# Kernel tuning notes

Measured on AMD Instinct MI355X. Metric: run time of the kernel, lower is better.

The kernel has to match this reference:

```python
import jax, jax.numpy as jnp
import numpy as np

NEG_SLOPE = 0.2  # PyG GATConv default leaky_relu slope
EPS = 1e-16


def gat_conv(x, W, att_src, att_dst, bias, src, dst, num_nodes, heads, out_ch, concat):
    # x: [N, F_in]; W: [F_in, heads*out_ch]
    h = (x @ W).reshape(num_nodes, heads, out_ch)          # [N, H, C]
    a_src = jnp.sum(h * att_src, axis=-1)                  # [N, H]
    a_dst = jnp.sum(h * att_dst, axis=-1)                  # [N, H]
    alpha = jax.nn.leaky_relu(a_src[src] + a_dst[dst], NEG_SLOPE)  # [E, H]
    # segment softmax over incoming edges of each destination node
    amax = jax.ops.segment_max(alpha, dst, num_segments=num_nodes)  # [N, H]
    ex = jnp.exp(alpha - amax[dst])                        # [E, H]
    denom = jax.ops.segment_sum(ex, dst, num_segments=num_nodes)    # [N, H]
    attn = ex / (denom[dst] + EPS)                         # [E, H]
    msg = h[src] * attn[:, :, None]                        # [E, H, C]
    out = jax.ops.segment_sum(msg, dst, num_segments=num_nodes)     # [N, H, C]
    if concat:
        out = out.reshape(num_nodes, heads * out_ch)
    else:
        out = out.mean(axis=1)
    return out + bias


def setup_inputs() -> dict:
    key = jax.random.key(0)
    ks = jax.random.split(key, 10)
    N, E, F_in, H, C, OUT = 50000, 800000, 512, 4, 64, 40
    x = jax.random.normal(ks[0], (N, F_in), dtype=jnp.float32)
    edge_index = jax.random.randint(ks[1], (2, E), 0, N, dtype=jnp.int64)
    s1 = (2.0 / (F_in + H * C)) ** 0.5
    s2 = (2.0 / (H * C + OUT)) ** 0.5
    return {
        "x": x,
        "edge_index": edge_index,
        "W1": jax.random.normal(ks[2], (F_in, H * C), dtype=jnp.float32) * s1,
        "att_src1": jax.random.normal(ks[3], (H, C), dtype=jnp.float32) * 0.1,
        "att_dst1": jax.random.normal(ks[4], (H, C), dtype=jnp.float32) * 0.1,
        "b1": jnp.zeros((H * C,), dtype=jnp.float32),
        "W2": jax.random.normal(ks[5], (H * C, OUT), dtype=jnp.float32) * s2,
        "att_src2": jax.random.normal(ks[6], (1, OUT), dtype=jnp.float32) * 0.1,
        "att_dst2": jax.random.normal(ks[7], (1, OUT), dtype=jnp.float32) * 0.1,
        "b2": jnp.zeros((OUT,), dtype=jnp.float32),
    }


def reference(x, edge_index, W1, att_src1, att_dst1, b1, W2, att_src2, att_dst2, b2):
    N = x.shape[0]
    H, C = att_src1.shape
    OUT = att_src2.shape[1]
    # PyG GATConv default: add self-loops
    loops = jnp.arange(N, dtype=edge_index.dtype)
    src = jnp.concatenate([edge_index[0], loops])
    dst = jnp.concatenate([edge_index[1], loops])
    # dropout is identity in eval mode
    h = gat_conv(x, W1, att_src1, att_dst1, b1, src, dst, N, H, C, concat=True)
    h = jax.nn.elu(h)
    out = gat_conv(h, W2, att_src2, att_dst2, b2, src, dst, N, 1, OUT, concat=False)
    return jax.nn.log_softmax(out, axis=1)
```

## Files before the change

### kernel.cpp

```cpp
#include <hip/hip_runtime.h>
#include <math.h>

#define FIN   512
#define H1DIM 256
#define HEADS 4
#define CH    64
#define OUTC  40
#define NEG   0.2f
#define EPSV  1e-16f
#define BK    64

__device__ __forceinline__ float leaky(float a) { return fmaxf(a, NEG * a); }

__device__ __forceinline__ short f2bf(float f) {
    unsigned u = __builtin_bit_cast(unsigned, f);
    u += 0x7FFFu + ((u >> 16) & 1u);
    return (short)(u >> 16);
}
__device__ __forceinline__ float bf2f(short s) {
    return __builtin_bit_cast(float, ((unsigned)(unsigned short)s) << 16);
}
__device__ __forceinline__ unsigned cvtpk(float lo, float hi) {
    unsigned r;
    asm("v_cvt_pk_bf16_f32 %0, %1, %2" : "=v"(r) : "v"(lo), "v"(hi));
    return r;
}
__device__ __forceinline__ float lo16(unsigned u) {
    return __builtin_bit_cast(float, u << 16);
}
__device__ __forceinline__ float hi16(unsigned u) {
    return __builtin_bit_cast(float, u & 0xffff0000u);
}

typedef __attribute__((ext_vector_type(2))) float floatx2;

__device__ __forceinline__ unsigned f32x2_to_fp8x2(float a, float b) {
    return (unsigned)__builtin_amdgcn_cvt_pk_fp8_f32(a, b, 0, false);
}
template <bool HI>
__device__ __forceinline__ floatx2 fp8x2_to_f32(unsigned u) {
    return __builtin_amdgcn_cvt_pk_f32_fp8((int)u, HI);
}

typedef __attribute__((ext_vector_type(8))) short short8;
typedef __attribute__((ext_vector_type(4))) short short4_t;
typedef __attribute__((ext_vector_type(4))) float float4_t;

typedef unsigned int u32;
typedef const __attribute__((address_space(1))) u32 gu32;
typedef __attribute__((address_space(3))) u32 lu32;

__device__ __forceinline__ void load_lds16(const void* g, void* l) {
    __builtin_amdgcn_global_load_lds((gu32*)g, (lu32*)l, 16, 0, 0);
}

__global__ void cvt_w1_kernel(const float* __restrict__ W1, short* __restrict__ w1t)
{
    int idx = blockIdx.x * 256 + threadIdx.x;
    if (idx >= FIN * H1DIM) return;
    int k = idx >> 8;
    int n = idx & 255;
    w1t[(size_t)n * FIN + k] = f2bf(W1[idx]);
}

__global__ __launch_bounds__(256) void gemm1_mfma_kernel(
    const float* __restrict__ x, const short* __restrict__ w1t,
    const float* __restrict__ attS, const float* __restrict__ attD,
    unsigned char* __restrict__ h1f, float* __restrict__ aS1, float* __restrict__ aD1, int N)
{
    __shared__ float Alf[64 * BK];
    __shared__ short Bls[256 * BK];

    const int tid  = threadIdx.x;
    const int lane = tid & 63;
    const int wid  = tid >> 6;
    const int row0 = blockIdx.x * 64;
    const int col0 = wid * 64;
    const int quad = lane >> 4;
    const int m16  = lane & 15;

    const int achunk = ((tid & 15) ^ (tid >> 4)) * 4;
    const float* asrcA[4];
#pragma unroll
    for (int p = 0; p < 4; ++p) {
        int r = row0 + p * 16 + (tid >> 4);
        if (r >= N) r = N - 1;
        asrcA[p] = x + (size_t)r * FIN + achunk;
    }

    const int trow = tid >> 3;
    const int bswz = ((tid & 7) ^ (trow & 7)) * 8;
    const short* bsrc[8];
#pragma unroll
    for (int p = 0; p < 8; ++p)
        bsrc[p] = w1t + (size_t)(p * 32 + trow) * FIN + bswz;

    float4_t acc[4][4];
#pragma unroll
    for (int i = 0; i < 4; ++i)
#pragma unroll
        for (int j = 0; j < 4; ++j) acc[i][j] = (float4_t){0.f, 0.f, 0.f, 0.f};

    const int swzB = (m16 & 7);

    for (int k0 = 0; k0 < FIN; k0 += BK) {
#pragma unroll
        for (int p = 0; p < 4; ++p)
            load_lds16(asrcA[p] + k0, Alf + p * 1024 + tid * 4);
#pragma unroll
        for (int p = 0; p < 8; ++p)
            load_lds16(bsrc[p] + k0, Bls + p * 2048 + tid * 8);
        __syncthreads();

#pragma unroll
        for (int half = 0; half < 2; ++half) {
            short8 a[4], b[4];
#pragma unroll
            for (int i = 0; i < 4; ++i) {
                int row = i * 16 + m16;
                int c0 = (quad + 4 * half) * 2;
                float4 f0 = *(const float4*)&Alf[row * BK + ((c0 ^ m16) * 4)];
                float4 f1 = *(const float4*)&Alf[row * BK + (((c0 + 1) ^ m16) * 4)];
                unsigned* tp = (unsigned*)&a[i];
                tp[0] = cvtpk(f0.x, f0.y);
                tp[1] = cvtpk(f0.z, f0.w);
                tp[2] = cvtpk(f1.x, f1.y);
                tp[3] = cvtpk(f1.z, f1.w);
            }
#pragma unroll
            for (int j = 0; j < 4; ++j) {
                int col = col0 + j * 16 + m16;
                int sub = (quad + 4 * half) ^ swzB;
                b[j] = *(const short8*)&Bls[col * BK + sub * 8];
            }
#pragma unroll
            for (int i = 0; i < 4; ++i)
#pragma unroll
                for (int j = 0; j < 4; ++j)
                    acc[i][j] = __builtin_amdgcn_mfma_f32_16x16x32_bf16(a[i], b[j], acc[i][j], 0, 0, 0);
        }
        __syncthreads();
    }

    float attSv[4], attDv[4];
#pragma unroll
    for (int j = 0; j < 4; ++j) {
        attSv[j] = attS[col0 + j * 16 + m16];
        attDv[j] = attD[col0 + j * 16 + m16];
    }

#pragma unroll
    for (int i = 0; i < 4; ++i) {
#pragma unroll
        for (int r = 0; r < 4; ++r) {
            int row = row0 + i * 16 + quad * 4 + r;
            if (row < N) {
                unsigned pa = f32x2_to_fp8x2(acc[i][0][r], acc[i][1][r]);
                unsigned pb = f32x2_to_fp8x2(acc[i][2][r], acc[i][3][r]);
                unsigned char* hp = h1f + (size_t)row * H1DIM + col0 + m16;
                hp[0]  = (unsigned char)(pa & 0xff);
                hp[16] = (unsigned char)((pa >> 8) & 0xff);
                hp[32] = (unsigned char)(pb & 0xff);
                hp[48] = (unsigned char)((pb >> 8) & 0xff);
            }
            float ps = acc[i][0][r] * attSv[0] + acc[i][1][r] * attSv[1]
                     + acc[i][2][r] * attSv[2] + acc[i][3][r] * attSv[3];
            float pd = acc[i][0][r] * attDv[0] + acc[i][1][r] * attDv[1]
                     + acc[i][2][r] * attDv[2] + acc[i][3][r] * attDv[3];
#pragma unroll
            for (int off = 1; off < 16; off <<= 1) {
                ps += __shfl_xor(ps, off);
                pd += __shfl_xor(pd, off);
            }
            if (m16 == 0 && row < N) {
                aS1[(size_t)row * 4 + wid] = ps;
                aD1[(size_t)row * 4 + wid] = pd;
            }
        }
    }
}

__global__ void degcount_kernel(const int* __restrict__ ei, int* __restrict__ deg,
                                int* __restrict__ rank, int E, int Etot)
{
    int e = blockIdx.x * 256 + threadIdx.x;
    if (e >= Etot) return;
    int d = (e < E) ? ei[E + e] : (e - E);
    rank[e] = atomicAdd(&deg[d], 1);
}

__global__ __launch_bounds__(1024) void scan_partial_kernel(
    const int* __restrict__ deg, int* __restrict__ offsets,
    int* __restrict__ bsums, int N)
{
    __shared__ int wsums[16];
    __shared__ int excl[16];
    int tid = threadIdx.x, lane = tid & 63, wid = tid >> 6;
    int idx = blockIdx.x * 1024 + tid;
    int v = (idx < N) ? deg[idx] : 0;
    int sv = v;
#pragma unroll
    for (int off = 1; off < 64; off <<= 1) {
        int t = __shfl_up(sv, off, 64);
        if (lane >= off) sv += t;
    }
    if (lane == 63) wsums[wid] = sv;
    __syncthreads();
    if (wid == 0 && lane < 16) {
        int wv = wsums[lane];
        int sw = wv;
#pragma unroll
        for (int off = 1; off < 16; off <<= 1) {
            int t = __shfl_up(sw, off, 64);
            if (lane >= off) sw += t;
        }
        excl[lane] = sw - wv;
        if (lane == 15) bsums[blockIdx.x] = sw;
    }
    __syncthreads();
    if (idx < N) offsets[idx + 1] = sv + excl[wid];
}

__global__ __launch_bounds__(1024) void scan_tops_kernel(
    int* __restrict__ bsums, int* __restrict__ boffs, int nb)
{
    __shared__ int wsums[16];
    __shared__ int excl[16];
    int tid = threadIdx.x, lane = tid & 63, wid = tid >> 6;
    int v = (tid < nb) ? bsums[tid] : 0;
    int sv = v;
#pragma unroll
    for (int off = 1; off < 64; off <<= 1) {
        int t = __shfl_up(sv, off, 64);
        if (lane >= off) sv += t;
    }
    if (lane == 63) wsums[wid] = sv;
    __syncthreads();
    if (wid == 0 && lane < 16) {
        int wv = wsums[lane];
        int sw = wv;
#pragma unroll
        for (int off = 1; off < 16; off <<= 1) {
            int t = __shfl_up(sw, off, 64);
            if (lane >= off) sw += t;
        }
        excl[lane] = sw - wv;
    }
    __syncthreads();
    if (tid < nb) boffs[tid] = sv + excl[wid] - v;
}

__global__ __launch_bounds__(1024) void scan_add_kernel(
    int* __restrict__ offsets, const int* __restrict__ boffs, int N)
{
    int idx = blockIdx.x * 1024 + threadIdx.x;
    if (idx == 0) offsets[0] = 0;
    if (idx < N) offsets[idx + 1] += boffs[blockIdx.x];
}

__global__ void scatter_kernel(const int* __restrict__ ei, const int* __restrict__ offsets,
                               const int* __restrict__ rank, int* __restrict__ csr_src,
                               int E, int Etot)
{
    int e = blockIdx.x * 256 + threadIdx.x;
    if (e >= Etot) return;
    int s, d;
    if (e < E) { s = ei[e]; d = ei[E + e]; }
    else       { s = e - E; d = s; }
    csr_src[offsets[d] + rank[e]] = s;
}

__global__ __launch_bounds__(256) void agg1_kernel(
    const unsigned char* __restrict__ h1f, const float* __restrict__ aS,
    const float* __restrict__ aD, const int* __restrict__ offsets,
    const int* __restrict__ csr_src, const float* __restrict__ b1,
    short* __restrict__ g1b, int N)
{
    int lane = threadIdx.x & 63, wid = threadIdx.x >> 6;
    int half = lane >> 5;
    int l32  = lane & 31;
    int n = blockIdx.x * 4 + wid;
    if (n >= N) return;
    int start = offsets[n], end = offsets[n + 1];
    int h = l32 >> 3;
    int cbase = l32 * 8;
    float adh = aD[(size_t)n * 4 + h];

    float ac[8];
#pragma unroll
    for (int c = 0; c < 8; ++c) ac[c] = 0.f;
    float denom = 0.f;

    int p = start;
    for (; p + 4 <= end; p += 4) {
        int sA0 = csr_src[p],     sB0 = csr_src[p + 1];
        int sA1 = csr_src[p + 2], sB1 = csr_src[p + 3];
        int s0 = half ? sB0 : sA0;
        int s1 = half ? sB1 : sA1;
        float t0 = aS[(size_t)s0 * 4 + h] + adh;
        float t1 = aS[(size_t)s1 * 4 + h] + adh;
        uint2 r0 = *(const uint2*)&h1f[(size_t)s0 * H1DIM + cbase];
        uint2 r1 = *(const uint2*)&h1f[(size_t)s1 * H1DIM + cbase];
        float w0 = __expf(leaky(t0));
        float w1 = __expf(leaky(t1));
        denom += w0 + w1;
        floatx2 d0a = fp8x2_to_f32<false>(r0.x), d0b = fp8x2_to_f32<true>(r0.x);
        floatx2 d0c = fp8x2_to_f32<false>(r0.y), d0d = fp8x2_to_f32<true>(r0.y);
        floatx2 d1a = fp8x2_to_f32<false>(r1.x), d1b = fp8x2_to_f32<true>(r1.x);
        floatx2 d1c = fp8x2_to_f32<false>(r1.y), d1d = fp8x2_to_f32<true>(r1.y);
        ac[0] += w0 * d0a.x + w1 * d1a.x;
        ac[1] += w0 * d0a.y + w1 * d1a.y;
        ac[2] += w0 * d0b.x + w1 * d1b.x;
        ac[3] += w0 * d0b.y + w1 * d1b.y;
        ac[4] += w0 * d0c.x + w1 * d1c.x;
        ac[5] += w0 * d0c.y + w1 * d1c.y;
        ac[6] += w0 * d0d.x + w1 * d1d.x;
        ac[7] += w0 * d0d.y + w1 * d1d.y;
    }
    for (; p + 2 <= end; p += 2) {
        int sA = csr_src[p], sB = csr_src[p + 1];
        int s = half ? sB : sA;
        float t = aS[(size_t)s * 4 + h] + adh;
        uint2 r = *(const uint2*)&h1f[(size_t)s * H1DIM + cbase];
        float w = __expf(leaky(t));
        denom += w;
        floatx2 da = fp8x2_to_f32<false>(r.x), db = fp8x2_to_f32<true>(r.x);
        floatx2 dc = fp8x2_to_f32<false>(r.y), dd = fp8x2_to_f32<true>(r.y);
        ac[0] += w * da.x; ac[1] += w * da.y;
        ac[2] += w * db.x; ac[3] += w * db.y;
        ac[4] += w * dc.x; ac[5] += w * dc.y;
        ac[6] += w * dd.x; ac[7] += w * dd.y;
    }
    if (p < end) {
        int s = csr_src[p];
        float t = aS[(size_t)s * 4 + h] + adh;
        uint2 r = *(const uint2*)&h1f[(size_t)s * H1DIM + cbase];
        float w = half ? 0.f : __expf(leaky(t));
        denom += w;
        floatx2 da = fp8x2_to_f32<false>(r.x), db = fp8x2_to_f32<true>(r.x);
        floatx2 dc = fp8x2_to_f32<false>(r.y), dd = fp8x2_to_f32<true>(r.y);
        ac[0] += w * da.x; ac[1] += w * da.y;
        ac[2] += w * db.x; ac[3] += w * db.y;
        ac[4] += w * dc.x; ac[5] += w * dc.y;
        ac[6] += w * dd.x; ac[7] += w * dd.y;
    }

    denom += __shfl_xor(denom, 32);
#pragma unroll
    for (int c = 0; c < 8; ++c) ac[c] += __shfl_xor(ac[c], 32);

    if (half == 0) {
        float inv = 1.f / (denom + EPSV);
        float4 b0 = *(const float4*)&b1[cbase];
        float4 b4 = *(const float4*)&b1[cbase + 4];
        float v[8];
        v[0] = ac[0] * inv + b0.x;
        v[1] = ac[1] * inv + b0.y;
        v[2] = ac[2] * inv + b0.z;
        v[3] = ac[3] * inv + b0.w;
        v[4] = ac[4] * inv + b4.x;
        v[5] = ac[5] * inv + b4.y;
        v[6] = ac[6] * inv + b4.z;
        v[7] = ac[7] * inv + b4.w;
#pragma unroll
        for (int c = 0; c < 8; ++c) v[c] = v[c] > 0.f ? v[c] : expm1f(v[c]);
        short8 o;
        unsigned* op = (unsigned*)&o;
        op[0] = cvtpk(v[0], v[1]);
        op[1] = cvtpk(v[2], v[3]);
        op[2] = cvtpk(v[4], v[5]);
        op[3] = cvtpk(v[6], v[7]);
        *(short8*)&g1b[(size_t)n * H1DIM + cbase] = o;
    }
}

__global__ __launch_bounds__(256) void gemm2_kernel(
    const short* __restrict__ g1b, const float* __restrict__ W2,
    const float* __restrict__ attS2, const float* __restrict__ attD2,
    short* __restrict__ h2b, float* __restrict__ aS2, float* __restrict__ aD2, int N)
{
    __shared__ float rows[4][8][256];
    int lane = threadIdx.x & 63, wid = threadIdx.x >> 6;
    int nbase = blockIdx.x * 32 + wid * 8;
    bool act = lane < OUTC;
    int cc = act ? lane : 0;
    float attS = act ? attS2[lane] : 0.f;
    float attD = act ? attD2[lane] : 0.f;

#pragma unroll
    for (int i = 0; i < 8; ++i) {
        int n = nbase + i;
        float4 v = make_float4(0.f, 0.f, 0.f, 0.f);
        if (n < N) {
            short4_t hv = *(const short4_t*)&g1b[(size_t)n * H1DIM + lane * 4];
            v = make_float4(bf2f(hv[0]), bf2f(hv[1]), bf2f(hv[2]), bf2f(hv[3]));
        }
        *(float4*)&rows[wid][i][lane * 4] = v;
    }

    float acc[8];
#pragma unroll
    for (int i = 0; i < 8; ++i) acc[i] = 0.f;

    for (int k = 0; k < H1DIM; k += 4) {
        float w0 = W2[(size_t)(k + 0) * OUTC + cc];
        float w1 = W2[(size_t)(k + 1) * OUTC + cc];
        float w2 = W2[(size_t)(k + 2) * OUTC + cc];
        float w3 = W2[(size_t)(k + 3) * OUTC + cc];
#pragma unroll
        for (int i = 0; i < 8; ++i) {
            float4 g = *(const float4*)&rows[wid][i][k];
            acc[i] += g.x * w0 + g.y * w1 + g.z * w2 + g.w * w3;
        }
    }

#pragma unroll
    for (int i = 0; i < 8; ++i) {
        int n = nbase + i;
        if (n >= N) continue;
        if (act) h2b[(size_t)n * OUTC + lane] = f2bf(acc[i]);
        float ts = act ? acc[i] * attS : 0.f;
        float td = act ? acc[i] * attD : 0.f;
#pragma unroll
        for (int off = 32; off > 0; off >>= 1) {
            ts += __shfl_xor(ts, off);
            td += __shfl_xor(td, off);
        }
        if (lane == 0) { aS2[n] = ts; aD2[n] = td; }
    }
}

__global__ __launch_bounds__(256) void agg2_kernel(
    const short* __restrict__ h2b, const float* __restrict__ aS2,
    const float* __restrict__ aD2, const int* __restrict__ offsets,
    const int* __restrict__ csr_src, const float* __restrict__ b2,
    float* __restrict__ out, int N)
{
    int lane = threadIdx.x & 63, wid = threadIdx.x >> 6;
    int n = blockIdx.x * 4 + wid;
    if (n >= N) return;
    int start = offsets[n], end = offsets[n + 1];
    bool act = lane < OUTC;
    int cc = act ? lane : 0;
    float ad = aD2[n];

    float acc = 0.f, denom = 0.f;
    int p = start;
    for (; p + 4 <= end; p += 4) {
        int s0 = csr_src[p], s1 = csr_src[p + 1], s2 = csr_src[p + 2], s3 = csr_src[p + 3];
        float w0 = __expf(leaky(aS2[s0] + ad));
        float w1 = __expf(leaky(aS2[s1] + ad));
        float w2 = __expf(leaky(aS2[s2] + ad));
        float w3 = __expf(leaky(aS2[s3] + ad));
        short v0 = h2b[(size_t)s0 * OUTC + cc];
        short v1 = h2b[(size_t)s1 * OUTC + cc];
        short v2 = h2b[(size_t)s2 * OUTC + cc];
        short v3 = h2b[(size_t)s3 * OUTC + cc];
        denom += w0 + w1 + w2 + w3;
        acc += w0 * bf2f(v0) + w1 * bf2f(v1) + w2 * bf2f(v2) + w3 * bf2f(v3);
    }
    for (; p < end; ++p) {
        int s = csr_src[p];
        float w = __expf(leaky(aS2[s] + ad));
        denom += w;
        acc += w * bf2f(h2b[(size_t)s * OUTC + cc]);
    }

    float v = acc / (denom + EPSV) + (act ? b2[lane] : 0.f);

    float vm = act ? v : -INFINITY;
#pragma unroll
    for (int off = 32; off > 0; off >>= 1) vm = fmaxf(vm, __shfl_xor(vm, off));
    float ex2 = act ? __expf(v - vm) : 0.f;
    float tot = ex2;
#pragma unroll
    for (int off = 32; off > 0; off >>= 1) tot += __shfl_xor(tot, off);
    float res = v - vm - __logf(tot);
    if (act) out[(size_t)n * OUTC + lane] = res;
}

extern "C" void kernel_launch(void* const* d_in, const int* in_sizes, int n_in,
                              void* d_out, int out_size, void* d_ws, size_t ws_size,
                              hipStream_t stream)
{
    const float* x     = (const float*)d_in[0];
    const int*   ei    = (const int*)d_in[1];
    const float* W1    = (const float*)d_in[2];
    const float* attS1 = (const float*)d_in[3];
    const float* attD1 = (const float*)d_in[4];
    const float* b1    = (const float*)d_in[5];
    const float* W2    = (const float*)d_in[6];
    const float* attS2 = (const float*)d_in[7];
    const float* attD2 = (const float*)d_in[8];
    const float* b2    = (const float*)d_in[9];
    float* out = (float*)d_out;

    const int N    = in_sizes[0] / FIN;
    const int E    = in_sizes[1] / 2;
    const int Etot = E + N;
    const int nb   = (N + 1023) / 1024;

    char* ws = (char*)d_ws;
    size_t off = 0;
    auto take = [&](size_t bytes) -> char* {
        char* p = ws + off;
        off = (off + bytes + 255) & ~(size_t)255;
        return p;
    };
    unsigned char* h1f = (unsigned char*)take((size_t)N * H1DIM);
    short* g1b     = (short*)take((size_t)N * H1DIM * 2);
    short* w1t     = (short*)take((size_t)FIN * H1DIM * 2);
    float* aS1     = (float*)take((size_t)N * 4 * 4);
    float* aD1     = (float*)take((size_t)N * 4 * 4);
    short* h2b     = (short*)take((size_t)N * OUTC * 2);
    float* aS2v    = (float*)take((size_t)N * 4);
    float* aD2v    = (float*)take((size_t)N * 4);
    int*   deg     = (int*)take((size_t)N * 4);
    int*   offsets = (int*)take((size_t)(N + 1) * 4);
    int*   bsums   = (int*)take((size_t)nb * 4);
    int*   boffs   = (int*)take((size_t)nb * 4);
    int*   rank    = (int*)take((size_t)Etot * 4);
    int*   csr_src = (int*)take((size_t)Etot * 4);

    (void)hipMemsetAsync(deg, 0, (size_t)N * 4, stream);

    cvt_w1_kernel<<<(FIN * H1DIM + 255) / 256, 256, 0, stream>>>(W1, w1t);
    gemm1_mfma_kernel<<<(N + 63) / 64, 256, 0, stream>>>(x, w1t, attS1, attD1, h1f, aS1, aD1, N);
    degcount_kernel<<<(Etot + 255) / 256, 256, 0, stream>>>(ei, deg, rank, E, Etot);
    scan_partial_kernel<<<nb, 1024, 0, stream>>>(deg, offsets, bsums, N);
    scan_tops_kernel<<<1, 1024, 0, stream>>>(bsums, boffs, nb);
    scan_add_kernel<<<nb, 1024, 0, stream>>>(offsets, boffs, N);
    scatter_kernel<<<(Etot + 255) / 256, 256, 0, stream>>>(ei, offsets, rank, csr_src, E, Etot);
    agg1_kernel<<<(N + 3) / 4, 256, 0, stream>>>(h1f, aS1, aD1, offsets, csr_src, b1, g1b, N);
    gemm2_kernel<<<(N + 31) / 32, 256, 0, stream>>>(g1b, W2, attS2, attD2, h2b, aS2v, aD2v, N);
    agg2_kernel<<<(N + 3) / 4, 256, 0, stream>>>(h2b, aS2v, aD2v, offsets, csr_src, b2, out, N);
}
```

Before: 389.4 us.

## Double-buffer A tile in LDS and load W1 fragments directly from global

The GEMM1 kernel drops the LDS staging of the bf16 W1 tile. Each lane now loads its B fragments straight from global memory, which W1's small size should keep in L2. The A (x) tile is double-buffered in LDS, with the next tile prefetched before the current one is computed, and manual vmcnt waits plus s_barrier replace __syncthreads. Launch bounds request 4 blocks per CU to raise occupancy, at the risk of register pressure and of uncoalesced B global loads with hand-tuned waitcnt values that must stay exact.

```diff
diff --git a/kernel.cpp b/kernel.cpp
--- a/kernel.cpp
+++ b/kernel.cpp
@@ -63,13 +63,12 @@
     w1t[(size_t)n * FIN + k] = f2bf(W1[idx]);
 }
 
-__global__ __launch_bounds__(256) void gemm1_mfma_kernel(
+__global__ __launch_bounds__(256, 4) void gemm1_mfma_kernel(
     const float* __restrict__ x, const short* __restrict__ w1t,
     const float* __restrict__ attS, const float* __restrict__ attD,
     unsigned char* __restrict__ h1f, float* __restrict__ aS1, float* __restrict__ aD1, int N)
 {
-    __shared__ float Alf[64 * BK];
-    __shared__ short Bls[256 * BK];
+    __shared__ float Alf[2][64 * BK];
 
     const int tid  = threadIdx.x;
     const int lane = tid & 63;
@@ -88,12 +87,10 @@
         asrcA[p] = x + (size_t)r * FIN + achunk;
     }
 
-    const int trow = tid >> 3;
-    const int bswz = ((tid & 7) ^ (trow & 7)) * 8;
-    const short* bsrc[8];
-#pragma unroll
-    for (int p = 0; p < 8; ++p)
-        bsrc[p] = w1t + (size_t)(p * 32 + trow) * FIN + bswz;
+    const short* bp[4];
+#pragma unroll
+    for (int j = 0; j < 4; ++j)
+        bp[j] = w1t + (size_t)(col0 + j * 16 + m16) * FIN + quad * 8;
 
     float4_t acc[4][4];
 #pragma unroll
@@ -101,26 +98,43 @@
 #pragma unroll
         for (int j = 0; j < 4; ++j) acc[i][j] = (float4_t){0.f, 0.f, 0.f, 0.f};
 
-    const int swzB = (m16 & 7);
-
-    for (int k0 = 0; k0 < FIN; k0 += BK) {
-#pragma unroll
-        for (int p = 0; p < 4; ++p)
-            load_lds16(asrcA[p] + k0, Alf + p * 1024 + tid * 4);
-#pragma unroll
-        for (int p = 0; p < 8; ++p)
-            load_lds16(bsrc[p] + k0, Bls + p * 2048 + tid * 8);
-        __syncthreads();
-
+#pragma unroll
+    for (int p = 0; p < 4; ++p)
+        load_lds16(asrcA[p], Alf[0] + p * 1024 + tid * 4);
+
+#pragma unroll
+    for (int kk = 0; kk < FIN / BK; ++kk) {
+        const int k0 = kk * BK;
+
+        short8 b[2][4];
+#pragma unroll
+        for (int half = 0; half < 2; ++half)
+#pragma unroll
+            for (int j = 0; j < 4; ++j)
+                b[half][j] = *(const short8*)(bp[j] + k0 + half * 32);
+
+        if (kk < FIN / BK - 1) {
+#pragma unroll
+            for (int p = 0; p < 4; ++p)
+                load_lds16(asrcA[p] + k0 + BK, Alf[(kk + 1) & 1] + p * 1024 + tid * 4);
+            asm volatile("s_waitcnt vmcnt(12)" ::: "memory");
+        } else {
+            asm volatile("s_waitcnt vmcnt(8)" ::: "memory");
+        }
+        __builtin_amdgcn_sched_barrier(0);
+        __builtin_amdgcn_s_barrier();
+        __builtin_amdgcn_sched_barrier(0);
+
+        const float* Acur = Alf[kk & 1];
 #pragma unroll
         for (int half = 0; half < 2; ++half) {
-            short8 a[4], b[4];
+            short8 a[4];
 #pragma unroll
             for (int i = 0; i < 4; ++i) {
                 int row = i * 16 + m16;
                 int c0 = (quad + 4 * half) * 2;
-                float4 f0 = *(const float4*)&Alf[row * BK + ((c0 ^ m16) * 4)];
-                float4 f1 = *(const float4*)&Alf[row * BK + (((c0 + 1) ^ m16) * 4)];
+                float4 f0 = *(const float4*)&Acur[row * BK + ((c0 ^ m16) * 4)];
+                float4 f1 = *(const float4*)&Acur[row * BK + (((c0 + 1) ^ m16) * 4)];
                 unsigned* tp = (unsigned*)&a[i];
                 tp[0] = cvtpk(f0.x, f0.y);
                 tp[1] = cvtpk(f0.z, f0.w);
@@ -128,18 +142,14 @@
                 tp[3] = cvtpk(f1.z, f1.w);
             }
 #pragma unroll
-            for (int j = 0; j < 4; ++j) {
-                int col = col0 + j * 16 + m16;
-                int sub = (quad + 4 * half) ^ swzB;
-                b[j] = *(const short8*)&Bls[col * BK + sub * 8];
-            }
-#pragma unroll
             for (int i = 0; i < 4; ++i)
 #pragma unroll
                 for (int j = 0; j < 4; ++j)
-                    acc[i][j] = __builtin_amdgcn_mfma_f32_16x16x32_bf16(a[i], b[j], acc[i][j], 0, 0, 0);
-        }
-        __syncthreads();
+                    acc[i][j] = __builtin_amdgcn_mfma_f32_16x16x32_bf16(a[i], b[half][j], acc[i][j], 0, 0, 0);
+        }
+        __builtin_amdgcn_sched_barrier(0);
+        __builtin_amdgcn_s_barrier();
+        __builtin_amdgcn_sched_barrier(0);
     }
 
     float attSv[4], attDv[4];
```

After: 411.1 us. +5.6%, slower.

## Double gemm1 row tile and stage fp8 output through LDS for coalesced stores

Applied to the files above, without the earlier changes.

The first-layer GEMM now computes 128 rows per block instead of 64, so each W1 tile loaded into LDS is reused across twice as many rows and fewer blocks are launched. The A-fragment conversion moves inside the row loop to keep register pressure down, and launch bounds request two blocks per SM. The fp8 outputs are written into an LDS bounce buffer and then stored as 16-byte vector writes instead of scattered single-byte stores. In exchange the kernel uses more accumulator registers and LDS per block, which may lower occupancy, and adds one extra barrier.

```diff
diff --git a/kernel.cpp b/kernel.cpp
--- a/kernel.cpp
+++ b/kernel.cpp
@@ -25,12 +25,6 @@
     asm("v_cvt_pk_bf16_f32 %0, %1, %2" : "=v"(r) : "v"(lo), "v"(hi));
     return r;
 }
-__device__ __forceinline__ float lo16(unsigned u) {
-    return __builtin_bit_cast(float, u << 16);
-}
-__device__ __forceinline__ float hi16(unsigned u) {
-    return __builtin_bit_cast(float, u & 0xffff0000u);
-}
 
 typedef __attribute__((ext_vector_type(2))) float floatx2;
 
@@ -63,26 +57,26 @@
     w1t[(size_t)n * FIN + k] = f2bf(W1[idx]);
 }
 
-__global__ __launch_bounds__(256) void gemm1_mfma_kernel(
+__global__ __launch_bounds__(256, 2) void gemm1_mfma_kernel(
     const float* __restrict__ x, const short* __restrict__ w1t,
     const float* __restrict__ attS, const float* __restrict__ attD,
     unsigned char* __restrict__ h1f, float* __restrict__ aS1, float* __restrict__ aD1, int N)
 {
-    __shared__ float Alf[64 * BK];
+    __shared__ float Alf[128 * BK];
     __shared__ short Bls[256 * BK];
 
     const int tid  = threadIdx.x;
     const int lane = tid & 63;
     const int wid  = tid >> 6;
-    const int row0 = blockIdx.x * 64;
+    const int row0 = blockIdx.x * 128;
     const int col0 = wid * 64;
     const int quad = lane >> 4;
     const int m16  = lane & 15;
 
     const int achunk = ((tid & 15) ^ (tid >> 4)) * 4;
-    const float* asrcA[4];
-#pragma unroll
-    for (int p = 0; p < 4; ++p) {
+    const float* asrcA[8];
+#pragma unroll
+    for (int p = 0; p < 8; ++p) {
         int r = row0 + p * 16 + (tid >> 4);
         if (r >= N) r = N - 1;
         asrcA[p] = x + (size_t)r * FIN + achunk;
@@ -95,9 +89,9 @@
     for (int p = 0; p < 8; ++p)
         bsrc[p] = w1t + (size_t)(p * 32 + trow) * FIN + bswz;
 
-    float4_t acc[4][4];
-#pragma unroll
-    for (int i = 0; i < 4; ++i)
+    float4_t acc[8][4];
+#pragma unroll
+    for (int i = 0; i < 8; ++i)
 #pragma unroll
         for (int j = 0; j < 4; ++j) acc[i][j] = (float4_t){0.f, 0.f, 0.f, 0.f};
 
@@ -105,7 +99,7 @@
 
     for (int k0 = 0; k0 < FIN; k0 += BK) {
 #pragma unroll
-        for (int p = 0; p < 4; ++p)
+        for (int p = 0; p < 8; ++p)
             load_lds16(asrcA[p] + k0, Alf + p * 1024 + tid * 4);
 #pragma unroll
         for (int p = 0; p < 8; ++p)
@@ -114,19 +108,7 @@
 
 #pragma unroll
         for (int half = 0; half < 2; ++half) {
-            short8 a[4], b[4];
-#pragma unroll
-            for (int i = 0; i < 4; ++i) {
-                int row = i * 16 + m16;
-                int c0 = (quad + 4 * half) * 2;
-                float4 f0 = *(const float4*)&Alf[row * BK + ((c0 ^ m16) * 4)];
-                float4 f1 = *(const float4*)&Alf[row * BK + (((c0 + 1) ^ m16) * 4)];
-                unsigned* tp = (unsigned*)&a[i];
-                tp[0] = cvtpk(f0.x, f0.y);
-                tp[1] = cvtpk(f0.z, f0.w);
-                tp[2] = cvtpk(f1.x, f1.y);
-                tp[3] = cvtpk(f1.z, f1.w);
-            }
+            short8 b[4];
 #pragma unroll
             for (int j = 0; j < 4; ++j) {
                 int col = col0 + j * 16 + m16;
@@ -134,10 +116,21 @@
                 b[j] = *(const short8*)&Bls[col * BK + sub * 8];
             }
 #pragma unroll
-            for (int i = 0; i < 4; ++i)
+            for (int i = 0; i < 8; ++i) {
+                int row = i * 16 + m16;
+                int c0 = (quad + 4 * half) * 2;
+                float4 f0 = *(const float4*)&Alf[row * BK + ((c0 ^ m16) * 4)];
+                float4 f1 = *(const float4*)&Alf[row * BK + (((c0 + 1) ^ m16) * 4)];
+                short8 a;
+                unsigned* tp = (unsigned*)&a;
+                tp[0] = cvtpk(f0.x, f0.y);
+                tp[1] = cvtpk(f0.z, f0.w);
+                tp[2] = cvtpk(f1.x, f1.y);
+                tp[3] = cvtpk(f1.z, f1.w);
 #pragma unroll
                 for (int j = 0; j < 4; ++j)
-                    acc[i][j] = __builtin_amdgcn_mfma_f32_16x16x32_bf16(a[i], b[j], acc[i][j], 0, 0, 0);
+                    acc[i][j] = __builtin_amdgcn_mfma_f32_16x16x32_bf16(a, b[j], acc[i][j], 0, 0, 0);
+            }
         }
         __syncthreads();
     }
@@ -149,20 +142,21 @@
         attDv[j] = attD[col0 + j * 16 + m16];
     }
 
-#pragma unroll
-    for (int i = 0; i < 4; ++i) {
+    unsigned char* Bounce = (unsigned char*)Alf;
+
+#pragma unroll
+    for (int i = 0; i < 8; ++i) {
 #pragma unroll
         for (int r = 0; r < 4; ++r) {
-            int row = row0 + i * 16 + quad * 4 + r;
-            if (row < N) {
-                unsigned pa = f32x2_to_fp8x2(acc[i][0][r], acc[i][1][r]);
-                unsigned pb = f32x2_to_fp8x2(acc[i][2][r], acc[i][3][r]);
-                unsigned char* hp = h1f + (size_t)row * H1DIM + col0 + m16;
-                hp[0]  = (unsigned char)(pa & 0xff);
-                hp[16] = (unsigned char)((pa >> 8) & 0xff);
-                hp[32] = (unsigned char)(pb & 0xff);
-                hp[48] = (unsigned char)((pb >> 8) & 0xff);
-            }
+            int rloc = i * 16 + quad * 4 + r;
+            unsigned pa = f32x2_to_fp8x2(acc[i][0][r], acc[i][1][r]);
+            unsigned pb = f32x2_to_fp8x2(acc[i][2][r], acc[i][3][r]);
+            int cb = rloc * 256 + col0 + m16;
+            Bounce[cb]      = (unsigned char)(pa & 0xff);
+            Bounce[cb + 16] = (unsigned char)((pa >> 8) & 0xff);
+            Bounce[cb + 32] = (unsigned char)(pb & 0xff);
+            Bounce[cb + 48] = (unsigned char)((pb >> 8) & 0xff);
+
             float ps = acc[i][0][r] * attSv[0] + acc[i][1][r] * attSv[1]
                      + acc[i][2][r] * attSv[2] + acc[i][3][r] * attSv[3];
             float pd = acc[i][0][r] * attDv[0] + acc[i][1][r] * attDv[1]
@@ -172,11 +166,21 @@
                 ps += __shfl_xor(ps, off);
                 pd += __shfl_xor(pd, off);
             }
+            int row = row0 + rloc;
             if (m16 == 0 && row < N) {
                 aS1[(size_t)row * 4 + wid] = ps;
                 aD1[(size_t)row * 4 + wid] = pd;
             }
         }
+    }
+    __syncthreads();
+
+#pragma unroll
+    for (int inst = 0; inst < 8; ++inst) {
+        int flat = inst * 4096 + tid * 16;
+        int row  = flat >> 8;
+        if (row0 + row < N)
+            *(float4*)(h1f + (size_t)row0 * H1DIM + flat) = *(const float4*)(Bounce + flat);
     }
 }
 
@@ -525,7 +529,7 @@
     (void)hipMemsetAsync(deg, 0, (size_t)N * 4, stream);
 
     cvt_w1_kernel<<<(FIN * H1DIM + 255) / 256, 256, 0, stream>>>(W1, w1t);
-    gemm1_mfma_kernel<<<(N + 63) / 64, 256, 0, stream>>>(x, w1t, attS1, attD1, h1f, aS1, aD1, N);
+    gemm1_mfma_kernel<<<(N + 127) / 128, 256, 0, stream>>>(x, w1t, attS1, attD1, h1f, aS1, aD1, N);
     degcount_kernel<<<(Etot + 255) / 256, 256, 0, stream>>>(ei, deg, rank, E, Etot);
     scan_partial_kernel<<<nb, 1024, 0, stream>>>(deg, offsets, bsums, N);
     scan_tops_kernel<<<1, 1024, 0, stream>>>(bsums, boffs, nb);
```

After: 389.4 us. About the same (+0.0%).
